# Optimization experiments

Measured on AMD Instinct MI355X. Metric: run time of the kernel, lower is better.

The kernel has to match this reference:

```python
import jax, jax.numpy as jnp
import numpy as np

B, T, C, H = 2, 2048, 1024, 16
HID = 4096
EPS = 1e-5
NEG_INF = float('-inf')


def layer_norm(x, w, b):
    mu = jnp.mean(x, axis=-1, keepdims=True)
    var = jnp.mean((x - mu) ** 2, axis=-1, keepdims=True)
    return (x - mu) / jnp.sqrt(var + EPS) * w + b


def setup_inputs() -> dict:
    key = jax.random.key(0)
    ks = jax.random.split(key, 12)
    s = lambda fan_in: 1.0 / np.sqrt(fan_in)
    return {
        'x': jax.random.normal(ks[0], (B, T, C), dtype=jnp.float32),
        'mask': jax.random.randint(ks[1], (B, T), 0, 2) > 0,
        'attn_w': jax.random.normal(ks[2], (C, 3 * C), dtype=jnp.float32) * s(C),
        'attn_b': jnp.zeros((3 * C,), dtype=jnp.float32),
        'proj_w': jax.random.normal(ks[3], (C, C), dtype=jnp.float32) * s(C),
        'proj_b': jnp.zeros((C,), dtype=jnp.float32),
        'ln1_w': jnp.ones((C,), dtype=jnp.float32),
        'ln1_b': jnp.zeros((C,), dtype=jnp.float32),
        'lin1_w': jax.random.normal(ks[4], (C, HID), dtype=jnp.float32) * s(C),
        'lin1_b': jnp.zeros((HID,), dtype=jnp.float32),
        'lin2_w': jax.random.normal(ks[5], (HID, C), dtype=jnp.float32) * s(HID),
        'lin2_b': jnp.zeros((C,), dtype=jnp.float32),
        'ln2_w': jnp.ones((C,), dtype=jnp.float32),
        'ln2_b': jnp.zeros((C,), dtype=jnp.float32),
    }


def reference(x, mask, attn_w, attn_b, proj_w, proj_b, ln1_w, ln1_b,
              lin1_w, lin1_b, lin2_w, lin2_b, ln2_w, ln2_b):
    D = C // H
    # fused QKV projection
    qkv = x @ attn_w + attn_b                      # [B,T,3C]
    q, k, v = jnp.split(qkv, 3, axis=-1)
    q = q.reshape(B, T, H, D).transpose(0, 2, 1, 3)  # [B,H,T,D]
    k = k.reshape(B, T, H, D).transpose(0, 2, 1, 3)
    v = v.reshape(B, T, H, D).transpose(0, 2, 1, 3)
    scale = 1.0 / jnp.sqrt(jnp.asarray(D, dtype=q.dtype))
    scores = jnp.einsum('bhqd,bhkd->bhqk', q, k) * scale  # [B,H,T,T]
    # bidirectional padding mask with forced-true first key column
    m2d = mask[:, None, :] & mask[:, :, None]       # [B,T,T]
    m2d = m2d.at[:, :, 0].set(True)
    bias = jnp.where(m2d, 0.0, NEG_INF).astype(scores.dtype)
    scores = scores + bias[:, None, :, :]
    w = jax.nn.softmax(scores, axis=-1)
    w = jnp.nan_to_num(w, nan=0.0, posinf=0.0, neginf=0.0)
    y = jnp.einsum('bhqk,bhkd->bhqd', w, v)
    y = y.transpose(0, 2, 1, 3).reshape(B, T, C)
    y = y @ proj_w + proj_b
    # residual + post-LN, then MLP + residual + post-LN
    h = layer_norm(x + y, ln1_w, ln1_b)
    ff = jax.nn.gelu(h @ lin1_w + lin1_b, approximate=False) @ lin2_w + lin2_b
    return layer_norm(h + ff, ln2_w, ln2_b)
```

## Files before the change

kernel.cpp:

```cpp
#include <hip/hip_runtime.h>
#include <hip/hip_bf16.h>
#include <math.h>

typedef __attribute__((ext_vector_type(4))) float f32x4;
typedef __attribute__((ext_vector_type(8))) __bf16 bf16x8v;
typedef __attribute__((ext_vector_type(4))) __bf16 bf16x4v;
typedef __attribute__((ext_vector_type(4))) short s16x4;
typedef __attribute__((ext_vector_type(4))) unsigned short u16x4;

#define AS1(p) ((const __attribute__((address_space(1))) void*)(p))
#define AS3(p) ((__attribute__((address_space(3))) void*)(p))

__device__ __forceinline__ unsigned short f2bf(float f) {
  union { __bf16 b; unsigned short u; } cv;
  cv.b = (__bf16)f;
  return cv.u;
}

__device__ __forceinline__ f32x4 mfma32(bf16x8v a, bf16x8v b, f32x4 c) {
  return __builtin_amdgcn_mfma_f32_16x16x32_bf16(a, b, c, 0, 0, 0);
}

__device__ __forceinline__ f32x4 mfma16(s16x4 a, s16x4 b, f32x4 c) {
#if __has_builtin(__builtin_amdgcn_mfma_f32_16x16x16bf16_1k)
  return __builtin_amdgcn_mfma_f32_16x16x16bf16_1k(a, b, c, 0, 0, 0);
#elif __has_builtin(__builtin_amdgcn_mfma_f32_16x16x16_bf16)
  bf16x4v av, bv;
  __builtin_memcpy(&av, &a, 8);
  __builtin_memcpy(&bv, &b, 8);
  return __builtin_amdgcn_mfma_f32_16x16x16_bf16(av, bv, c, 0, 0, 0);
#else
  asm volatile("v_mfma_f32_16x16x16_bf16 %0, %1, %2, %0\n\ts_nop 7\n\ts_nop 7\n\ts_nop 7"
               : "+v"(c) : "v"(a), "v"(b));
  return c;
#endif
}

__device__ __forceinline__ void async_copy16(const void* g, void* l) {
  __builtin_amdgcn_global_load_lds(AS1(g), AS3(l), 16, 0, 0);
}

__global__ __launch_bounds__(256) void cvt_bf16_kernel(const float* __restrict__ in,
                                                       unsigned short* __restrict__ out, int n4) {
  int i = blockIdx.x * 256 + threadIdx.x;
  if (i < n4) {
    f32x4 v = ((const f32x4*)in)[i];
    u16x4 o;
    o.x = f2bf(v.x); o.y = f2bf(v.y); o.z = f2bf(v.z); o.w = f2bf(v.w);
    ((u16x4*)out)[i] = o;
  }
}

__global__ __launch_bounds__(256) void wtrans_kernel(const float* __restrict__ W,
                                                     unsigned short* __restrict__ Wt,
                                                     int Kd, int Nd) {
  __shared__ float t[32][33];
  int tx = threadIdx.x & 31, ty = threadIdx.x >> 5;
  int bx = blockIdx.x, by = blockIdx.y;
  for (int i = 0; i < 4; ++i) {
    int r = by * 32 + ty + i * 8, c = bx * 32 + tx;
    t[ty + i * 8][tx] = W[(size_t)r * Nd + c];
  }
  __syncthreads();
  for (int i = 0; i < 4; ++i) {
    int nn = bx * 32 + ty + i * 8, kk = by * 32 + tx;
    Wt[(size_t)nn * Kd + kk] = f2bf(t[tx][ty + i * 8]);
  }
}

template <int EPI>
__global__ __launch_bounds__(256) void gemm_bt(const unsigned short* __restrict__ A,
                                               const unsigned short* __restrict__ Bt,
                                               const float* __restrict__ bias,
                                               void* __restrict__ out,
                                               unsigned short* __restrict__ outQ,
                                               unsigned short* __restrict__ outK,
                                               unsigned short* __restrict__ outV,
                                               int M, int N, int Kd, int gx) {
  __shared__ __align__(16) unsigned short As[3][128 * 32];
  __shared__ __align__(16) unsigned short Bs[3][128 * 32];
  int tid = threadIdx.x, wid = tid >> 6, lane = tid & 63;
  int lo = lane & 15, hi = lane >> 4;

  int wg = blockIdx.x, nwg = gridDim.x;
  int cpx = nwg >> 3;
  int swz = (wg & 7) * cpx + (wg >> 3);
  int m0 = (swz / gx) * 128, n0 = (swz % gx) * 128;

  int wm = wid >> 1, wn = wid & 1;
  f32x4 acc[4][4];
  for (int m = 0; m < 4; ++m)
    for (int n = 0; n < 4; ++n) acc[m][n] = f32x4{0.f, 0.f, 0.f, 0.f};
  int sr = lane >> 2;
  int sc = (lane & 3) * 8;
  int nkt = Kd >> 5;

  auto stage = [&](int buf, int kt) {
    int k0 = kt * 32;
#pragma unroll
    for (int i = 0; i < 2; ++i) {
      int ch = wid * 2 + i;
      const unsigned short* ga = A + ((size_t)(m0 + ch * 16 + sr)) * Kd + k0 + sc;
      async_copy16(ga, &As[buf][ch * 512]);
      const unsigned short* gb = Bt + ((size_t)(n0 + ch * 16 + sr)) * Kd + k0 + sc;
      async_copy16(gb, &Bs[buf][ch * 512]);
    }
  };

  stage(0, 0);
  stage(1, 1);
  stage(2, 2);
  int cur = 0;
  for (int kt = 0; kt < nkt; ++kt) {
    asm volatile("s_waitcnt vmcnt(8)" ::: "memory");
    asm volatile("s_barrier" ::: "memory");
    __builtin_amdgcn_sched_barrier(0);
    bf16x8v af[4], bf_[4];
#pragma unroll
    for (int m = 0; m < 4; ++m)
      af[m] = *(const bf16x8v*)&As[cur][(wm * 64 + m * 16 + lo) * 32 + hi * 8];
#pragma unroll
    for (int n = 0; n < 4; ++n)
      bf_[n] = *(const bf16x8v*)&Bs[cur][(wn * 64 + n * 16 + lo) * 32 + hi * 8];
#pragma unroll
    for (int m = 0; m < 4; ++m)
#pragma unroll
      for (int n = 0; n < 4; ++n)
        acc[m][n] = mfma32(af[m], bf_[n], acc[m][n]);
    __builtin_amdgcn_sched_barrier(0);
    asm volatile("s_barrier" ::: "memory");
    int nx = kt + 3;
    nx = nx < nkt ? nx : nkt - 1;
    stage(cur, nx);
    cur = cur + 1;
    cur = cur == 3 ? 0 : cur;
  }

#pragma unroll
  for (int n = 0; n < 4; ++n) {
    int col = n0 + wn * 64 + n * 16 + lo;
    float bv = bias ? bias[col] : 0.f;
#pragma unroll
    for (int m = 0; m < 4; ++m) {
      int row0 = m0 + wm * 64 + m * 16 + hi * 4;
#pragma unroll
      for (int j = 0; j < 4; ++j) {
        float v = acc[m][n][j] + bv;
        int row = row0 + j;
        size_t idx = (size_t)row * N + col;
        if (EPI == 0) {
          ((unsigned short*)out)[idx] = f2bf(v);
        } else if (EPI == 1) {
          ((float*)out)[idx] = v;
        } else if (EPI == 2) {
          float g = 0.5f * v * (1.f + erff(v * 0.70710678118654752f));
          ((unsigned short*)out)[idx] = f2bf(g);
        } else {
          int c2 = col & 1023, h = c2 >> 6, d = c2 & 63;
          int bq = row >> 11, t = row & 2047;
          unsigned short val = f2bf(v);
          if (col < 2048) {
            unsigned short* dst = (col < 1024) ? outQ : outK;
            dst[(((size_t)(bq * 16 + h)) * 2048 + t) * 64 + d] = val;
          } else {
            outV[(((size_t)(bq * 16 + h)) * 64 + d) * 2048 + t] = val;
          }
        }
      }
    }
  }
}

__global__ __launch_bounds__(256) void attn_kernel(const unsigned short* __restrict__ Q,
                                                   const unsigned short* __restrict__ Kt,
                                                   const unsigned short* __restrict__ Vt,
                                                   const int* __restrict__ mask,
                                                   unsigned short* __restrict__ Y) {
  __shared__ __align__(16) unsigned short Kl[2][4096];
  __shared__ __align__(16) unsigned short Vl[2][4096];
  __shared__ float sbias[2048];

  int qt = blockIdx.x, bh = blockIdx.y;
  int b = bh >> 4, h = bh & 15;
  int tid = threadIdx.x, wv = tid >> 6, lane = tid & 63;
  int lo = lane & 15, hi = lane >> 4;

  for (int k = tid; k < 2048; k += 256) {
    int mk = mask[b * 2048 + k];
    sbias[k] = (mk != 0 || k == 0) ? 0.f : -1e30f;
  }

  int r8 = lane >> 3;
  int jsrc = (((lane & 7) ^ r8) << 4);
  const size_t kvbase = (size_t)bh * 2048;

  auto stage = [&](int buf, int kt2) {
    int kbase = kt2 * 64;
#pragma unroll
    for (int i = 0; i < 2; ++i) {
      int r = i * 32 + wv * 8 + r8;
      const unsigned short* gk = Kt + (kvbase + kbase + r) * 64 + (jsrc >> 1);
      async_copy16(gk, (char*)Kl + buf * 8192 + i * 4096 + wv * 1024);
      const unsigned short* gv = Vt + ((size_t)bh * 64 + r) * 2048 + kbase + (jsrc >> 1);
      async_copy16(gv, (char*)Vl + buf * 8192 + i * 4096 + wv * 1024);
    }
  };

  int qrow = qt * 64 + wv * 16 + lo;
  size_t qoff = (kvbase + qrow) * 64;
  bf16x8v Qf0 = *(const bf16x8v*)(Q + qoff + hi * 8);
  bf16x8v Qf1 = *(const bf16x8v*)(Q + qoff + 32 + hi * 8);
  float qm = (mask[b * 2048 + qrow] != 0) ? -16.f : -1e30f;

  const float scale2 = 0.125f * 1.44269504088896340736f;
  float l_run = 0.f;
  f32x4 acc[4];
#pragma unroll
  for (int c = 0; c < 4; ++c) acc[c] = f32x4{0.f, 0.f, 0.f, 0.f};

  stage(0, 0);
  stage(1, 1);
  asm volatile("s_waitcnt lgkmcnt(0)" ::: "memory");

  int sw = (lo & 7) << 4;
  int cur = 0;
  for (int kt = 0; kt < 32; ++kt) {
    asm volatile("s_waitcnt vmcnt(4)" ::: "memory");
    asm volatile("s_barrier" ::: "memory");
    __builtin_amdgcn_sched_barrier(0);
    int kbase = kt * 64;

    f32x4 s4[4];
#pragma unroll
    for (int kb = 0; kb < 4; ++kb) {
      const char* kr = (const char*)Kl + cur * 8192 + (kb * 16 + lo) * 128;
      bf16x8v K0 = *(const bf16x8v*)(kr + ((hi * 16) ^ sw));
      bf16x8v K1 = *(const bf16x8v*)(kr + ((64 + hi * 16) ^ sw));
      f32x4 z = f32x4{0.f, 0.f, 0.f, 0.f};
      z = mfma32(K0, Qf0, z);
      z = mfma32(K1, Qf1, z);
      s4[kb] = z;
    }

    float p[16];
#pragma unroll
    for (int kb = 0; kb < 4; ++kb) {
      f32x4 bb = *(const f32x4*)&sbias[kbase + kb * 16 + hi * 4];
#pragma unroll
      for (int r = 0; r < 4; ++r)
        p[kb * 4 + r] = fmaf(s4[kb][r], scale2, bb[r] + qm);
    }
    if (kt == 0)
      p[0] = (hi == 0) ? fmaf(s4[0][0], scale2, -16.f) : p[0];
#pragma unroll
    for (int i = 0; i < 16; ++i) p[i] = exp2f(p[i]);
    float ls0 = 0.f, ls1 = 0.f;
#pragma unroll
    for (int i = 0; i < 8; ++i) { ls0 += p[i]; ls1 += p[8 + i]; }
    l_run += ls0 + ls1;

    union { __bf16 b[4]; s16x4 s4v; } pk[4];
#pragma unroll
    for (int kb = 0; kb < 4; ++kb)
#pragma unroll
      for (int r = 0; r < 4; ++r) pk[kb].b[r] = (__bf16)p[kb * 4 + r];

#pragma unroll
    for (int c = 0; c < 4; ++c) {
      const char* vr = (const char*)Vl + cur * 8192 + (c * 16 + lo) * 128;
#pragma unroll
      for (int kk = 0; kk < 4; ++kk) {
        s16x4 V0 = *(const s16x4*)(vr + ((kk * 32 + hi * 8) ^ sw));
        acc[c] = mfma16(V0, pk[kk].s4v, acc[c]);
      }
    }
    __builtin_amdgcn_sched_barrier(0);
    asm volatile("s_barrier" ::: "memory");
    int nx = kt + 2;
    nx = nx < 32 ? nx : 31;
    stage(cur, nx);
    cur ^= 1;
  }

  l_run += __shfl_xor(l_run, 16);
  l_run += __shfl_xor(l_run, 32);
  float invl = 1.f / l_run;
  size_t yrow = ((size_t)(b * 2048 + qrow)) * 1024 + h * 64;
#pragma unroll
  for (int c = 0; c < 4; ++c)
#pragma unroll
    for (int r = 0; r < 4; ++r)
      Y[yrow + c * 16 + hi * 4 + r] = f2bf(acc[c][r] * invl);
}

__global__ __launch_bounds__(256) void ln_kernel(const float* __restrict__ A,
                                                 const float* __restrict__ Bsrc,
                                                 const float* __restrict__ w,
                                                 const float* __restrict__ bias,
                                                 float* __restrict__ outF,
                                                 unsigned short* __restrict__ outB) {
  int row = blockIdx.x, tid = threadIdx.x;
  f32x4 r = ((const f32x4*)A)[row * 256 + tid] + ((const f32x4*)Bsrc)[row * 256 + tid];
  float s = r.x + r.y + r.z + r.w;
  float q = r.x * r.x + r.y * r.y + r.z * r.z + r.w * r.w;
  for (int off = 1; off < 64; off <<= 1) {
    s += __shfl_xor(s, off);
    q += __shfl_xor(q, off);
  }
  __shared__ float ls[4], lq[4];
  int wid = tid >> 6, lane = tid & 63;
  if (lane == 0) { ls[wid] = s; lq[wid] = q; }
  __syncthreads();
  s = ls[0] + ls[1] + ls[2] + ls[3];
  q = lq[0] + lq[1] + lq[2] + lq[3];
  float mu = s * (1.f / 1024.f);
  float var = q * (1.f / 1024.f) - mu * mu;
  float rstd = rsqrtf(var + 1e-5f);
  f32x4 wv = ((const f32x4*)w)[tid];
  f32x4 bv = ((const f32x4*)bias)[tid];
  f32x4 o = (r - mu) * rstd * wv + bv;
  if (outF) ((f32x4*)outF)[row * 256 + tid] = o;
  if (outB) {
    u16x4 ob;
    ob.x = f2bf(o.x); ob.y = f2bf(o.y); ob.z = f2bf(o.z); ob.w = f2bf(o.w);
    ((u16x4*)outB)[row * 256 + tid] = ob;
  }
}

extern "C" void kernel_launch(void* const* d_in, const int* in_sizes, int n_in,
                              void* d_out, int out_size, void* d_ws, size_t ws_size,
                              hipStream_t stream) {
  const float* x      = (const float*)d_in[0];
  const int*   mask   = (const int*)d_in[1];
  const float* attn_w = (const float*)d_in[2];
  const float* attn_b = (const float*)d_in[3];
  const float* proj_w = (const float*)d_in[4];
  const float* proj_b = (const float*)d_in[5];
  const float* ln1_w  = (const float*)d_in[6];
  const float* ln1_b  = (const float*)d_in[7];
  const float* lin1_w = (const float*)d_in[8];
  const float* lin1_b = (const float*)d_in[9];
  const float* lin2_w = (const float*)d_in[10];
  const float* lin2_b = (const float*)d_in[11];
  const float* ln2_w  = (const float*)d_in[12];
  const float* ln2_b  = (const float*)d_in[13];
  float* out = (float*)d_out;

  char* ws = (char*)d_ws;
  size_t off = 0;
  auto alloc = [&](size_t bytes) { char* p = ws + off; off += (bytes + 255) & ~(size_t)255; return p; };

  unsigned short* attn_wT = (unsigned short*)alloc((size_t)3072 * 1024 * 2);
  unsigned short* proj_wT = (unsigned short*)alloc((size_t)1024 * 1024 * 2);
  unsigned short* lin1_wT = (unsigned short*)alloc((size_t)4096 * 1024 * 2);
  unsigned short* lin2_wT = (unsigned short*)alloc((size_t)1024 * 4096 * 2);
  char* regionA = alloc((size_t)3 * 8388608);
  char* regionB = alloc((size_t)8388608);
  char* regionC = alloc((size_t)25165824);
  float* h_f32  = (float*)alloc((size_t)4096 * 1024 * 4);
  unsigned short* h_bf16 = (unsigned short*)alloc((size_t)4096 * 1024 * 2);
  float* mlp2   = (float*)alloc((size_t)4096 * 1024 * 4);

  unsigned short* Qb  = (unsigned short*)regionA;
  unsigned short* Kb  = (unsigned short*)(regionA + 8388608);
  unsigned short* Vtb = (unsigned short*)(regionA + 16777216);
  unsigned short* ff1 = (unsigned short*)regionA;
  unsigned short* xb  = (unsigned short*)regionB;
  unsigned short* Yb  = (unsigned short*)regionC;
  float* proj_out     = (float*)(regionC + 8388608);

  wtrans_kernel<<<dim3(96, 32), 256, 0, stream>>>(attn_w, attn_wT, 1024, 3072);
  wtrans_kernel<<<dim3(32, 32), 256, 0, stream>>>(proj_w, proj_wT, 1024, 1024);
  wtrans_kernel<<<dim3(128, 32), 256, 0, stream>>>(lin1_w, lin1_wT, 1024, 4096);
  wtrans_kernel<<<dim3(32, 128), 256, 0, stream>>>(lin2_w, lin2_wT, 4096, 1024);
  cvt_bf16_kernel<<<4096, 256, 0, stream>>>(x, xb, 4096 * 1024 / 4);

  gemm_bt<3><<<768, 256, 0, stream>>>(xb, attn_wT, attn_b, nullptr, Qb, Kb, Vtb,
                                      4096, 3072, 1024, 24);

  attn_kernel<<<dim3(32, 32), 256, 0, stream>>>(Qb, Kb, Vtb, mask, Yb);

  gemm_bt<1><<<256, 256, 0, stream>>>(Yb, proj_wT, proj_b, proj_out, nullptr, nullptr, nullptr,
                                      4096, 1024, 1024, 8);
  ln_kernel<<<4096, 256, 0, stream>>>(x, proj_out, ln1_w, ln1_b, h_f32, h_bf16);

  gemm_bt<2><<<1024, 256, 0, stream>>>(h_bf16, lin1_wT, lin1_b, ff1, nullptr, nullptr, nullptr,
                                       4096, 4096, 1024, 32);
  gemm_bt<1><<<256, 256, 0, stream>>>(ff1, lin2_wT, lin2_b, mlp2, nullptr, nullptr, nullptr,
                                      4096, 1024, 4096, 8);
  ln_kernel<<<4096, 256, 0, stream>>>(h_f32, mlp2, ln2_w, ln2_b, out, nullptr);
}
```

Before: 441.4 us.

## Add 256x256 GEMM kernel for QKV and MLP1, split QKV scatter into reshape kernels

Adds a 512-thread GEMM using 256x256 tiles with BK=64, swizzled LDS and double buffering. It replaces the 128x128 kernel for the QKV projection and the first MLP projection, aiming for more data reuse per tile. The QKV epilogue no longer scatters into head layout. The GEMM writes a plain row-major qkv buffer, and separate reshape and V-transpose kernels then build Q, K and Vt. This adds two extra launches and an extra round trip of the QKV activations through memory. The 192 and 256 workgroup grids may also underfill the 256 CUs.

```diff
diff --git a/kernel.cpp b/kernel.cpp
--- a/kernel.cpp
+++ b/kernel.cpp
@@ -69,13 +69,105 @@
 }
 
 template <int EPI>
+__global__ __launch_bounds__(512, 2) void gemm256(const unsigned short* __restrict__ A,
+                                                  const unsigned short* __restrict__ Bt,
+                                                  const float* __restrict__ bias,
+                                                  unsigned short* __restrict__ out,
+                                                  int M, int N, int Kd, int gx) {
+  __shared__ __align__(16) unsigned short Al[2][256 * 64];
+  __shared__ __align__(16) unsigned short Bl[2][256 * 64];
+  int tid = threadIdx.x, wid = tid >> 6, lane = tid & 63;
+  int lo = lane & 15, hi = lane >> 4;
+  int wm = wid >> 2, wn = wid & 3;
+
+  int wg = blockIdx.x, nwg = gridDim.x;
+  int cpx = nwg >> 3;
+  int swz = (wg & 7) * cpx + (wg >> 3);
+  int m0 = (swz / gx) * 256, n0 = (swz % gx) * 256;
+
+  f32x4 acc[8][4];
+#pragma unroll
+  for (int mf = 0; mf < 8; ++mf)
+#pragma unroll
+    for (int nf = 0; nf < 4; ++nf) acc[mf][nf] = f32x4{0.f, 0.f, 0.f, 0.f};
+
+  int nkt = Kd >> 6;
+
+  auto stageAB = [&](int buf, int kt) {
+#pragma unroll
+    for (int i = 0; i < 4; ++i) {
+      int G = (wid * 4 + i) * 64 + lane;
+      int row = G >> 3, c16 = G & 7;
+      int csw = ((c16 ^ (row & 7)) << 3);
+      const unsigned short* ga = A + ((size_t)(m0 + row)) * Kd + kt * 64 + csw;
+      async_copy16(ga, &Al[buf][(wid * 4 + i) * 512]);
+      const unsigned short* gb = Bt + ((size_t)(n0 + row)) * Kd + kt * 64 + csw;
+      async_copy16(gb, &Bl[buf][(wid * 4 + i) * 512]);
+    }
+  };
+
+  stageAB(0, 0);
+  int cur = 0;
+  for (int t = 0; t < nkt; ++t) {
+    __builtin_amdgcn_s_barrier();
+    int nx = t + 1 < nkt ? t + 1 : nkt - 1;
+    stageAB(cur ^ 1, nx);
+    asm volatile("s_waitcnt vmcnt(8)" ::: "memory");
+    __builtin_amdgcn_sched_barrier(0);
+
+    bf16x8v bfr[4][2];
+#pragma unroll
+    for (int nf = 0; nf < 4; ++nf) {
+      int rb = wn * 64 + nf * 16 + lo;
+#pragma unroll
+      for (int kh = 0; kh < 2; ++kh)
+        bfr[nf][kh] = *(const bf16x8v*)&Bl[cur][rb * 64 + (((kh * 4 + hi) ^ (rb & 7)) << 3)];
+    }
+#pragma unroll
+    for (int q = 0; q < 4; ++q) {
+      bf16x8v afr[2][2];
+#pragma unroll
+      for (int m2 = 0; m2 < 2; ++m2) {
+        int ra = wm * 128 + (q * 2 + m2) * 16 + lo;
+#pragma unroll
+        for (int kh = 0; kh < 2; ++kh)
+          afr[m2][kh] = *(const bf16x8v*)&Al[cur][ra * 64 + (((kh * 4 + hi) ^ (ra & 7)) << 3)];
+      }
+      __builtin_amdgcn_s_setprio(1);
+#pragma unroll
+      for (int m2 = 0; m2 < 2; ++m2)
+#pragma unroll
+        for (int nf = 0; nf < 4; ++nf) {
+          acc[q * 2 + m2][nf] = mfma32(afr[m2][0], bfr[nf][0], acc[q * 2 + m2][nf]);
+          acc[q * 2 + m2][nf] = mfma32(afr[m2][1], bfr[nf][1], acc[q * 2 + m2][nf]);
+        }
+      __builtin_amdgcn_s_setprio(0);
+    }
+    cur ^= 1;
+  }
+
+#pragma unroll
+  for (int nf = 0; nf < 4; ++nf) {
+    int col = n0 + wn * 64 + nf * 16 + lo;
+    float bv = bias[col];
+#pragma unroll
+    for (int mf = 0; mf < 8; ++mf) {
+      int row0 = m0 + wm * 128 + mf * 16 + hi * 4;
+#pragma unroll
+      for (int j = 0; j < 4; ++j) {
+        float v = acc[mf][nf][j] + bv;
+        if (EPI == 2) v = 0.5f * v * (1.f + erff(v * 0.70710678118654752f));
+        out[(size_t)(row0 + j) * N + col] = f2bf(v);
+      }
+    }
+  }
+}
+
+template <int EPI>
 __global__ __launch_bounds__(256) void gemm_bt(const unsigned short* __restrict__ A,
                                                const unsigned short* __restrict__ Bt,
                                                const float* __restrict__ bias,
                                                void* __restrict__ out,
-                                               unsigned short* __restrict__ outQ,
-                                               unsigned short* __restrict__ outK,
-                                               unsigned short* __restrict__ outV,
                                                int M, int N, int Kd, int gx) {
   __shared__ __align__(16) unsigned short As[3][128 * 32];
   __shared__ __align__(16) unsigned short Bs[3][128 * 32];
@@ -146,28 +238,45 @@
 #pragma unroll
       for (int j = 0; j < 4; ++j) {
         float v = acc[m][n][j] + bv;
-        int row = row0 + j;
-        size_t idx = (size_t)row * N + col;
-        if (EPI == 0) {
-          ((unsigned short*)out)[idx] = f2bf(v);
-        } else if (EPI == 1) {
-          ((float*)out)[idx] = v;
-        } else if (EPI == 2) {
-          float g = 0.5f * v * (1.f + erff(v * 0.70710678118654752f));
-          ((unsigned short*)out)[idx] = f2bf(g);
-        } else {
-          int c2 = col & 1023, h = c2 >> 6, d = c2 & 63;
-          int bq = row >> 11, t = row & 2047;
-          unsigned short val = f2bf(v);
-          if (col < 2048) {
-            unsigned short* dst = (col < 1024) ? outQ : outK;
-            dst[(((size_t)(bq * 16 + h)) * 2048 + t) * 64 + d] = val;
-          } else {
-            outV[(((size_t)(bq * 16 + h)) * 64 + d) * 2048 + t] = val;
-          }
-        }
+        size_t idx = (size_t)(row0 + j) * N + col;
+        if (EPI == 1) ((float*)out)[idx] = v;
+        else          ((unsigned short*)out)[idx] = f2bf(v);
       }
     }
+  }
+}
+
+__global__ __launch_bounds__(256) void reshape_qk_kernel(const unsigned short* __restrict__ qkv,
+                                                         unsigned short* __restrict__ Q,
+                                                         unsigned short* __restrict__ K) {
+  int idx = blockIdx.x * 256 + threadIdx.x;
+  int row = idx >> 9;
+  int g = idx & 511;
+  int col = g * 4;
+  int sec = col >> 10;
+  int cc = col & 1023;
+  int h = cc >> 6, d = cc & 63;
+  int b = row >> 11, t = row & 2047;
+  u16x4 v = *(const u16x4*)&qkv[(size_t)row * 3072 + col];
+  unsigned short* dst = sec ? K : Q;
+  *(u16x4*)&dst[(((size_t)(b * 16 + h)) * 2048 + t) * 64 + d] = v;
+}
+
+__global__ __launch_bounds__(256) void vtrans_kernel(const unsigned short* __restrict__ qkv,
+                                                     unsigned short* __restrict__ Vt) {
+  __shared__ unsigned short t[32][33];
+  int tx = threadIdx.x & 31, ty = threadIdx.x >> 5;
+  int bx = blockIdx.x, dt = blockIdx.y, bh = blockIdx.z;
+  int b = bh >> 4, h = bh & 15;
+  for (int i = 0; i < 4; ++i) {
+    int trow = bx * 32 + ty + i * 8;
+    t[ty + i * 8][tx] = qkv[((size_t)(b * 2048 + trow)) * 3072 + 2048 + h * 64 + dt * 32 + tx];
+  }
+  __syncthreads();
+  for (int i = 0; i < 4; ++i) {
+    int d = dt * 32 + ty + i * 8;
+    int trow = bx * 32 + tx;
+    Vt[((size_t)bh * 64 + d) * 2048 + trow] = t[tx][ty + i * 8];
   }
 }
 
@@ -366,6 +475,7 @@
   unsigned short* Vtb = (unsigned short*)(regionA + 16777216);
   unsigned short* ff1 = (unsigned short*)regionA;
   unsigned short* xb  = (unsigned short*)regionB;
+  unsigned short* qkv = (unsigned short*)regionC;
   unsigned short* Yb  = (unsigned short*)regionC;
   float* proj_out     = (float*)(regionC + 8388608);
 
@@ -375,18 +485,16 @@
   wtrans_kernel<<<dim3(32, 128), 256, 0, stream>>>(lin2_w, lin2_wT, 4096, 1024);
   cvt_bf16_kernel<<<4096, 256, 0, stream>>>(x, xb, 4096 * 1024 / 4);
 
-  gemm_bt<3><<<768, 256, 0, stream>>>(xb, attn_wT, attn_b, nullptr, Qb, Kb, Vtb,
-                                      4096, 3072, 1024, 24);
+  gemm256<0><<<192, 512, 0, stream>>>(xb, attn_wT, attn_b, qkv, 4096, 3072, 1024, 12);
+  reshape_qk_kernel<<<8192, 256, 0, stream>>>(qkv, Qb, Kb);
+  vtrans_kernel<<<dim3(64, 2, 32), 256, 0, stream>>>(qkv, Vtb);
 
   attn_kernel<<<dim3(32, 32), 256, 0, stream>>>(Qb, Kb, Vtb, mask, Yb);
 
-  gemm_bt<1><<<256, 256, 0, stream>>>(Yb, proj_wT, proj_b, proj_out, nullptr, nullptr, nullptr,
-                                      4096, 1024, 1024, 8);
+  gemm_bt<1><<<256, 256, 0, stream>>>(Yb, proj_wT, proj_b, proj_out, 4096, 1024, 1024, 8);
   ln_kernel<<<4096, 256, 0, stream>>>(x, proj_out, ln1_w, ln1_b, h_f32, h_bf16);
 
-  gemm_bt<2><<<1024, 256, 0, stream>>>(h_bf16, lin1_wT, lin1_b, ff1, nullptr, nullptr, nullptr,
-                                       4096, 4096, 1024, 32);
-  gemm_bt<1><<<256, 256, 0, stream>>>(ff1, lin2_wT, lin2_b, mlp2, nullptr, nullptr, nullptr,
-                                      4096, 1024, 4096, 8);
+  gemm256<2><<<256, 512, 0, stream>>>(h_bf16, lin1_wT, lin1_b, ff1, 4096, 4096, 1024, 16);
+  gemm_bt<1><<<256, 256, 0, stream>>>(ff1, lin2_wT, lin2_b, mlp2, 4096, 1024, 4096, 8);
   ln_kernel<<<4096, 256, 0, stream>>>(h_f32, mlp2, ln2_w, ln2_b, out, nullptr);
 }
```

After: 440.7 us. Within noise of the previous version (-0.2%).
